# Kernel tuning notes

Measured on AMD Instinct MI355X. Metric: run time of the kernel, lower is better.

The kernel has to match this reference:

```python
import jax, jax.numpy as jnp
import numpy as np

B, NA, NB, E = 2, 256, 256, 512
H1, H2 = 300, 100


def setup_inputs() -> dict:
    key = jax.random.key(0)
    ks = jax.random.split(key, 16)

    def n(k, shape, scale=1.0):
        return jax.random.normal(k, shape, dtype=jnp.float32) * scale

    z = lambda shape: jnp.zeros(shape, jnp.float32)
    return {
        "action_embedding": n(ks[0], (B, E, NA)),
        "anchor_embedding": n(ks[1], (B, E, NB)),
        "action_points": n(ks[2], (B, 3, NA)),
        "anchor_points": n(ks[3], (B, 3, NB)),
        # pairwise MLP kernel params: 2E -> 300 -> 100 -> 1
        "mlp_W1": n(ks[4], (2 * E, H1), (2 * E) ** -0.5),
        "mlp_b1": z((H1,)),
        "mlp_W2": n(ks[5], (H1, H2), H1 ** -0.5),
        "mlp_b2": z((H2,)),
        "mlp_W3": n(ks[6], (H2, 1), H2 ** -0.5),
        "mlp_b3": z((1,)),
        # PointNet [512,64,64,64,128,512] (1x1 convs) + Conv1d(512,1,bias=False)
        "pn_W0": n(ks[7], (64, 512), 512 ** -0.5),
        "pn_b0": z((64,)),
        "pn_W1": n(ks[8], (64, 64), 64 ** -0.5),
        "pn_b1": z((64,)),
        "pn_W2": n(ks[9], (64, 64), 64 ** -0.5),
        "pn_b2": z((64,)),
        "pn_W3": n(ks[10], (128, 64), 64 ** -0.5),
        "pn_b3": z((128,)),
        "pn_W4": n(ks[11], (512, 128), 128 ** -0.5),
        "pn_b4": z((512,)),
        "head_W": n(ks[12], (1, 512), 512 ** -0.5),
    }


def reference(action_embedding, anchor_embedding, action_points, anchor_points,
              mlp_W1, mlp_b1, mlp_W2, mlp_b2, mlp_W3, mlp_b3,
              pn_W0, pn_b0, pn_W1, pn_b1, pn_W2, pn_b2, pn_W3, pn_b3,
              pn_W4, pn_b4, head_W):
    P_A = action_points.transpose(0, 2, 1)      # (B, NA, 3)
    P_B = anchor_points.transpose(0, 2, 1)      # (B, NB, 3)
    Phi_A = action_embedding.transpose(0, 2, 1)  # (B, NA, E)
    Phi_B = anchor_embedding.transpose(0, 2, 1)  # (B, NB, E)
    Ed = Phi_A.shape[-1]

    # --- symmetric pairwise MLP kernel: softplus((mlp(cat(a,b)) + mlp(cat(b,a))) / 2) ---
    # First Linear layer is split so the O(NA*NB*2E) concat is never materialized:
    # cat(a,b) @ W1 == a @ W1[:E] + b @ W1[E:]
    W1a, W1b = mlp_W1[:Ed], mlp_W1[Ed:]

    def mlp_tail(h):  # h: (B, NA, NB, H1) pre-activation of layer 1
        h = jax.nn.relu(h)
        h = jax.nn.relu(h @ mlp_W2 + mlp_b2)
        return (h @ mlp_W3 + mlp_b3)[..., 0]  # (B, NA, NB)

    hA_a = Phi_A @ W1a  # (B, NA, H1)
    hA_b = Phi_A @ W1b
    hB_a = Phi_B @ W1a  # (B, NB, H1)
    hB_b = Phi_B @ W1b
    v1 = mlp_tail(hA_a[:, :, None, :] + hB_b[:, None, :, :] + mlp_b1)  # mlp(cat(x1,x2))
    v2 = mlp_tail(hB_a[:, None, :, :] + hA_b[:, :, None, :] + mlp_b1)  # mlp(cat(x2,x1))
    R_est = jax.nn.softplus((v1 + v2) * 0.5)  # (B, NA, NB) estimated distances

    # --- weighted multilateration (estimate_p), vectorized over (B, NA) ---
    # Linearized LS: ||p||^2 - 2 q_k^T p = r_k^2 - ||q_k||^2; subtract weighted means
    # to eliminate ||p||^2, then solve 3x3 weighted normal equations per action point.
    w = jnp.ones(P_B.shape[:2], R_est.dtype)            # (B, NB) uniform weights (last_attn=False)
    wsum = w.sum(-1, keepdims=True)                      # (B, 1)
    qbar = (w[..., None] * P_B).sum(1) / wsum            # (B, 3)
    bvec = (P_B ** 2).sum(-1)[:, None, :] - R_est ** 2   # (B, NA, NB)
    bbar = (w[:, None, :] * bvec).sum(-1) / wsum         # (B, NA)
    Amat = 2.0 * (P_B - qbar[:, None, :])                # (B, NB, 3)
    yvec = bvec - bbar[..., None]                        # (B, NA, NB)
    M = jnp.einsum('bki,bk,bkj->bij', Amat, w, Amat)     # (B, 3, 3)
    rhs = jnp.einsum('bki,bk,bak->bai', Amat, w, yvec)   # (B, NA, 3)
    P_A_B_pred = jnp.linalg.solve(M[:, None], rhs[..., None])[..., 0]  # (B, NA, 3)

    flow = (P_A_B_pred - P_A).transpose(0, 2, 1)         # (B, 3, NA)

    # --- PointNet flow-weight head (1x1 convs + ReLU, final conv no bias) ---
    x = action_embedding                                  # (B, 512, NA)
    for Wc, bc in ((pn_W0, pn_b0), (pn_W1, pn_b1), (pn_W2, pn_b2),
                   (pn_W3, pn_b3), (pn_W4, pn_b4)):
        x = jax.nn.relu(jnp.einsum('oi,bin->bon', Wc, x) + bc[None, :, None])
    weight = jnp.einsum('oi,bin->bon', head_W, x)        # (B, 1, NA)

    full_flow = jnp.concatenate([flow, weight], axis=1)  # (B, 4, NA)
    return full_flow
```

## Files before the change

### kernel.cpp

```cpp
#include <hip/hip_runtime.h>
#include <hip/hip_bf16.h>
#include <hip/hip_fp16.h>

typedef float f32x4 __attribute__((ext_vector_type(4)));
typedef float f32x16 __attribute__((ext_vector_type(16)));
typedef short s16x8 __attribute__((ext_vector_type(8)));
typedef _Float16 f16x8 __attribute__((ext_vector_type(8)));

#define OFF_EMBT   0u
#define OFF_W1T    1048576u
#define OFF_W2TSW  1662976u
#define OFF_W0BF   1740800u
#define OFF_HA     1806336u
#define OFF_R2     3051520u
#define OFF_PNPK   3575808u
#define WS_TOTAL   3739648u

__device__ __forceinline__ int pack_bf2(float a, float b) {
  __hip_bfloat162 h = __float22bfloat162_rn(make_float2(a, b));
  int r; __builtin_memcpy(&r, &h, 4); return r;
}
__device__ __forceinline__ unsigned pack_f16_2(float a, float b) {
  __half2 h = __float22half2_rn(make_float2(a, b));
  unsigned r; __builtin_memcpy(&r, &h, 4); return r;
}
__device__ __forceinline__ unsigned short bf16u(float f) {
  __hip_bfloat16 h = __float2bfloat16(f);
  unsigned short u; __builtin_memcpy(&u, &h, 2); return u;
}
template<int CTRL>
__device__ __forceinline__ float dpp_add(float x) {
  int xi; __builtin_memcpy(&xi, &x, 4);
  int yi = __builtin_amdgcn_update_dpp(0, xi, CTRL, 0xf, 0xf, true);
  float y; __builtin_memcpy(&y, &yi, 4);
  return x + y;
}
__device__ __forceinline__ float swz_xor16(float x) {
  int xi; __builtin_memcpy(&xi, &x, 4);
  int yi = __builtin_amdgcn_ds_swizzle(xi, 0x401f);
  float y; __builtin_memcpy(&y, &yi, 4);
  return y;
}

__global__ __launch_bounds__(256) void ka_prep(
    const float* __restrict__ act_emb, const float* __restrict__ anc_emb,
    const float* __restrict__ W1, const float* __restrict__ W2,
    const float* __restrict__ W0pn,
    const float* __restrict__ pnW1, const float* __restrict__ pnW2,
    const float* __restrict__ pnW3, const float* __restrict__ pnW4,
    char* __restrict__ ws)
{
  __hip_bfloat16* embT  = (__hip_bfloat16*)(ws + OFF_EMBT);
  __hip_bfloat16* W1T   = (__hip_bfloat16*)(ws + OFF_W1T);
  unsigned short* W2Tsw = (unsigned short*)(ws + OFF_W2TSW);
  unsigned short* W0bf  = (unsigned short*)(ws + OFF_W0BF);
  __shared__ float tile[64][65];
  int blk = blockIdx.x, t = threadIdx.x;
  if (blk < 128) {
    int b = blk >> 6, emb = (blk >> 5) & 1, ntile = (blk >> 3) & 3, etile = blk & 7;
    const float* src = emb ? anc_emb : act_emb;
    int e0 = etile * 64, n0 = ntile * 64;
    int rr = t >> 6, cc = t & 63;
    #pragma unroll
    for (int it2 = 0; it2 < 16; ++it2) {
      int e_l = rr * 16 + it2;
      tile[e_l][cc] = src[(size_t)(b * 512 + e0 + e_l) * 256 + n0 + cc];
    }
    __syncthreads();
    int n_l = t >> 2, eq = t & 3;
    unsigned int* dst = (unsigned int*)(embT + ((size_t)((b * 2 + emb) * 256 + n0 + n_l)) * 512 + e0 + eq * 16);
    #pragma unroll
    for (int kk = 0; kk < 8; ++kk)
      dst[kk] = (unsigned)pack_bf2(tile[eq * 16 + 2 * kk][n_l], tile[eq * 16 + 2 * kk + 1][n_l]);
  } else if (blk < 208) {
    int id = blk - 128;
    int half = id / 40; int rem = id % 40; int et = rem / 5; int ct = rem % 5;
    int e0 = et * 64, c0 = ct * 64;
    int rr = t >> 6, cc = t & 63;
    #pragma unroll
    for (int it2 = 0; it2 < 16; ++it2) {
      int e_l = rr * 16 + it2;
      int c = c0 + cc;
      tile[e_l][cc] = (c < 300) ? W1[(size_t)(half * 512 + e0 + e_l) * 300 + c] : 0.f;
    }
    __syncthreads();
    int c_l = t >> 2, eq = t & 3;
    if (c0 + c_l < 300) {
      unsigned int* dst = (unsigned int*)(W1T + ((size_t)(half * 300 + c0 + c_l)) * 512 + e0 + eq * 16);
      #pragma unroll
      for (int kk = 0; kk < 8; ++kk)
        dst[kk] = (unsigned)pack_bf2(tile[eq * 16 + 2 * kk][c_l], tile[eq * 16 + 2 * kk + 1][c_l]);
    }
  } else if (blk < 227) {
    int idx = (blk - 208) * 256 + t;
    int lane = idx & 63; int ntks = idx >> 6; int nt = ntks & 3; int ks = ntks >> 2;
    int n = nt * 32 + (lane & 31);
    int kb = ks * 16 + (lane >> 5) * 8;
    unsigned int q[4];
    #pragma unroll
    for (int jj = 0; jj < 4; ++jj) {
      int k0 = kb + jj * 2, k1 = kb + jj * 2 + 1;
      float f0 = (n < 100 && k0 < 300) ? W2[(size_t)k0 * 100 + n] : 0.f;
      float f1 = (n < 100 && k1 < 300) ? W2[(size_t)k1 * 100 + n] : 0.f;
      q[jj] = pack_f16_2(f0, f1);
    }
    ((uint4*)W2Tsw)[idx] = make_uint4(q[0], q[1], q[2], q[3]);
  } else if (blk < 243) {
    int idx = (blk - 227) * 256 + t;
    const float* s = W0pn + (size_t)idx * 8;
    ((uint4*)W0bf)[idx] = make_uint4(
        (unsigned)pack_bf2(s[0], s[1]), (unsigned)pack_bf2(s[2], s[3]),
        (unsigned)pack_bf2(s[4], s[5]), (unsigned)pack_bf2(s[6], s[7]));
  } else if (blk < 247) {
    int idx = (blk - 243) * 256 + t;
    _Float16* haf = (_Float16*)(ws + OFF_HA);
    #pragma unroll
    for (int u2 = 0; u2 < 2; ++u2) {
      int unit = idx * 2 + u2;
      int combo = unit >> 5, row = unit & 31;
      size_t off = (((size_t)combo * 19 + 18) << 9) + (1 << 8) + (row << 3) + 4;
      unsigned* p = (unsigned*)(haf + off);
      p[0] = 0u; p[1] = 0u;
    }
  } else {
    int idx = (blk - 247) * 256 + t;
    const float* s;
    if (idx < 512)       s = pnW1 + (size_t)idx * 8;
    else if (idx < 1024) s = pnW2 + (size_t)(idx - 512) * 8;
    else if (idx < 2048) s = pnW3 + (size_t)(idx - 1024) * 8;
    else                 s = pnW4 + (size_t)(idx - 2048) * 8;
    unsigned short* pnPK = (unsigned short*)(ws + OFF_PNPK);
    ((uint4*)pnPK)[idx] = make_uint4(
        (unsigned)pack_bf2(s[0], s[1]), (unsigned)pack_bf2(s[2], s[3]),
        (unsigned)pack_bf2(s[4], s[5]), (unsigned)pack_bf2(s[6], s[7]));
  }
}

template<int K, int NT>
__device__ __forceinline__ void pn_layer(unsigned short* xb, const unsigned short* __restrict__ Wp,
                                         const float* __restrict__ bias, int wv, int l, int g)
{
  constexpr int NN = NT / 4;
  f32x4 z = {0.f, 0.f, 0.f, 0.f};
  f32x4 acc[NN];
  #pragma unroll
  for (int nn = 0; nn < NN; ++nn) acc[nn] = z;
  #pragma unroll
  for (int nn = 0; nn < NN; ++nn) {
    int o = (wv + nn * 4) * 16 + l;
    const unsigned short* wr0 = Wp + (size_t)o * K;
    #pragma unroll
    for (int ks = 0; ks < K / 32; ++ks) {
      int koff = ks * 32 + g * 8;
      s16x8 bfr = *(const s16x8*)(wr0 + koff);
      s16x8 a0 = *(const s16x8*)(xb + (size_t)l * 520 + koff);
      acc[nn] = __builtin_amdgcn_mfma_f32_16x16x32_bf16(a0, bfr, acc[nn], 0, 0, 0);
    }
  }
  __syncthreads();
  #pragma unroll
  for (int nn = 0; nn < NN; ++nn) {
    int chan = (wv + nn * 4) * 16 + l;
    float bv = bias[chan];
    #pragma unroll
    for (int r = 0; r < 4; ++r)
      xb[(size_t)(g * 4 + r) * 520 + chan] = bf16u(fmaxf(acc[nn][r] + bv, 0.f));
  }
  __syncthreads();
}

__global__ __launch_bounds__(256) void k1_ha(
    const __hip_bfloat16* __restrict__ embT, const __hip_bfloat16* __restrict__ W1T,
    const float* __restrict__ b1, _Float16* __restrict__ ha_f,
    const unsigned short* __restrict__ W0bf, const unsigned short* __restrict__ pnPK,
    const float* __restrict__ pnB0, const float* __restrict__ pnB1,
    const float* __restrict__ pnB2, const float* __restrict__ pnB3,
    const float* __restrict__ pnB4,
    const float* __restrict__ headW, float* __restrict__ out)
{
  __shared__ unsigned short xbuf[16 * 520];
  int blk = blockIdx.x, t = threadIdx.x;
  int wv = t >> 6, lane = t & 63, l = lane & 15, g = lane >> 4;
  if (blk < 320) {
    int b = blk / 160; int r = blk % 160; int emb = r / 80; r %= 80;
    int mch = r / 5; int nch = r % 5;
    int m0 = mch * 16;
    const unsigned short* Ap = (const unsigned short*)embT +
        ((size_t)((b * 2 + emb) * 256 + m0 + l)) * 512;
    const unsigned short* Wp = (const unsigned short*)W1T;
    f32x4 z = {0.f, 0.f, 0.f, 0.f};
    f32x4 acc[2] = {z, z};
    for (int ks = 0; ks < 16; ++ks) {
      int k0 = ks * 32 + g * 8;
      s16x8 af = *(const s16x8*)(Ap + k0);
      #pragma unroll
      for (int q = 0; q < 2; ++q) {
        int c = nch * 120 + (wv * 2 + q) * 16 + l;
        s16x8 bf = {0, 0, 0, 0, 0, 0, 0, 0};
        if (c < 600) bf = *(const s16x8*)(Wp + (size_t)c * 512 + k0);
        acc[q] = __builtin_amdgcn_mfma_f32_16x16x32_bf16(af, bf, acc[q], 0, 0, 0);
      }
    }
    #pragma unroll
    for (int q = 0; q < 2; ++q) {
      int cl = (wv * 2 + q) * 16 + l;
      int c = nch * 120 + cl;
      if (cl < 120 && c < 600) {
        int half = (c >= 300) ? 1 : 0;
        int cc = c - half * 300;
        float bias = (emb == 0) ? b1[cc] : 0.f;
        int d = emb * 2 + half;
        int ksf = cc >> 4, hi2 = (cc >> 3) & 1, e = cc & 7;
        #pragma unroll
        for (int r2 = 0; r2 < 4; ++r2) {
          int i = m0 + g * 4 + r2;
          size_t off = (((((size_t)(b * 4 + d)) * 8 + (i >> 5)) * 19 + ksf) << 9)
                     + (hi2 << 8) + ((i & 31) << 3) + e;
          ha_f[off] = (_Float16)__float2half_rn(acc[q][r2] + bias);
        }
      }
    }
  } else {
    int pn = blk - 320;
    int b_pn = pn >> 4, n0 = (pn & 15) * 16;
    unsigned short* xb = xbuf;
    {
      const unsigned short* A0 = (const unsigned short*)embT + ((size_t)(b_pn * 2 * 256 + n0)) * 512;
      f32x4 acc0 = {0.f, 0.f, 0.f, 0.f};
      int o = wv * 16 + l;
      const unsigned short* w0r = W0bf + (size_t)o * 512;
      #pragma unroll
      for (int ks = 0; ks < 16; ++ks) {
        int koff = ks * 32 + g * 8;
        s16x8 bfr = *(const s16x8*)(w0r + koff);
        s16x8 a0 = *(const s16x8*)(A0 + (size_t)l * 512 + koff);
        acc0 = __builtin_amdgcn_mfma_f32_16x16x32_bf16(a0, bfr, acc0, 0, 0, 0);
      }
      float bv = pnB0[o];
      #pragma unroll
      for (int r2 = 0; r2 < 4; ++r2)
        xb[(size_t)(g * 4 + r2) * 520 + o] = bf16u(fmaxf(acc0[r2] + bv, 0.f));
      __syncthreads();
    }
    pn_layer<64, 4>(xb, pnPK, pnB1, wv, l, g);
    pn_layer<64, 4>(xb, pnPK + 4096, pnB2, wv, l, g);
    pn_layer<64, 8>(xb, pnPK + 8192, pnB3, wv, l, g);
    pn_layer<128, 32>(xb, pnPK + 16384, pnB4, wv, l, g);
    {
      int p_l = t >> 4, os = t & 15;
      const unsigned short* row = xb + (size_t)p_l * 520 + os * 32;
      float s = 0.f;
      #pragma unroll
      for (int c = 0; c < 32; ++c) {
        unsigned int u = ((unsigned int)row[c]) << 16;
        float xv; __builtin_memcpy(&xv, &u, 4);
        s += xv * headW[os * 32 + c];
      }
      s += __shfl_xor(s, 1); s += __shfl_xor(s, 2);
      s += __shfl_xor(s, 4); s += __shfl_xor(s, 8);
      if (os == 0) out[(size_t)(b_pn * 4 + 3) * 256 + n0 + p_l] = s;
    }
  }
}

__global__ __launch_bounds__(512, 2) void k2_main(
    const _Float16* __restrict__ haF, const unsigned short* __restrict__ W2Tsw,
    const float* __restrict__ b2g, const float* __restrict__ W3g, const float* __restrict__ b3g,
    float* __restrict__ R2)
{
  __shared__ int4 w2s[4864];
  __shared__ float ex[4][2][2][16];
  int blkp = blockIdx.x, t = threadIdx.x;
  int blk = (blkp & 7) * 64 + (blkp >> 3);
  int wv = t >> 6, lane = t & 63, col = lane & 31, hi = lane >> 5;
  int jl = wv & 3, nh = wv >> 2;
  int u = blk; int b = u >> 8; u &= 255; int it = u >> 5; int jtp = u & 31;
  int i0 = it * 32;
  int j0 = jtp * 8 + jl * 2;
  {
    const int4* w2g = (const int4*)W2Tsw;
    #pragma unroll
    for (int q = 0; q < 9; ++q) { int idx = t + q * 512; w2s[idx] = w2g[idx]; }
    { int idx = t + 9 * 512; if (idx < 4864) w2s[idx] = w2g[idx]; }
  }
  const _Float16* pA0 = haF + ((((size_t)(b * 4 + 0)) * 8 + it) * 19) * 512 + lane * 8;
  const _Float16* pA1 = haF + ((((size_t)(b * 4 + 1)) * 8 + it) * 19) * 512 + lane * 8;
  const _Float16* pB00 = haF + ((((size_t)(b * 4 + 3)) * 8 + (j0 >> 5)) * 19) * 512
                         + (hi * 32 + (j0 & 31)) * 8;
  const _Float16* pB10 = haF + ((((size_t)(b * 4 + 2)) * 8 + (j0 >> 5)) * 19) * 512
                         + (hi * 32 + (j0 & 31)) * 8;
  f16x8 a0c = *(const f16x8*)(pA0);
  f16x8 a1c = *(const f16x8*)(pA1);
  f16x8 b00c = *(const f16x8*)(pB00);
  f16x8 b01c = *(const f16x8*)(pB00 + 8);
  f16x8 b10c = *(const f16x8*)(pB10);
  f16x8 b11c = *(const f16x8*)(pB10 + 8);
  __syncthreads();

  const f16x8 zf = {0, 0, 0, 0, 0, 0, 0, 0};
  f32x16 z16;
  #pragma unroll
  for (int q = 0; q < 16; ++q) z16[q] = 0.f;
  f32x16 aJ0D0N0 = z16, aJ0D0N1 = z16, aJ0D1N0 = z16, aJ0D1N1 = z16;
  f32x16 aJ1D0N0 = z16, aJ1D0N1 = z16, aJ1D1N0 = z16, aJ1D1N1 = z16;

  #pragma unroll 1
  for (int ks = 0; ks < 19; ++ks) {
    f16x8 a0n, a1n, b00n, b01n, b10n, b11n;
    if (ks < 18) {
      int ko = (ks + 1) * 512;
      a0n = *(const f16x8*)(pA0 + ko);
      a1n = *(const f16x8*)(pA1 + ko);
      b00n = *(const f16x8*)(pB00 + ko);
      b01n = *(const f16x8*)(pB00 + ko + 8);
      b10n = *(const f16x8*)(pB10 + ko);
      b11n = *(const f16x8*)(pB10 + ko + 8);
    } else { a0n = a0c; a1n = a1c; b00n = b00c; b01n = b01c; b10n = b10c; b11n = b11c; }
    f16x8 af00 = __builtin_elementwise_max(a0c + b00c, zf);
    f16x8 af01 = __builtin_elementwise_max(a0c + b01c, zf);
    f16x8 af10 = __builtin_elementwise_max(a1c + b10c, zf);
    f16x8 af11 = __builtin_elementwise_max(a1c + b11c, zf);
    const int4* wp = &w2s[ks * 256 + nh * 128 + lane];
    f16x8 wf0 = *(const f16x8*)(wp);
    f16x8 wf1 = *(const f16x8*)(wp + 64);
    aJ0D0N0 = __builtin_amdgcn_mfma_f32_32x32x16_f16(af00, wf0, aJ0D0N0, 0, 0, 0);
    aJ1D0N0 = __builtin_amdgcn_mfma_f32_32x32x16_f16(af01, wf0, aJ1D0N0, 0, 0, 0);
    aJ0D1N0 = __builtin_amdgcn_mfma_f32_32x32x16_f16(af10, wf0, aJ0D1N0, 0, 0, 0);
    aJ1D1N0 = __builtin_amdgcn_mfma_f32_32x32x16_f16(af11, wf0, aJ1D1N0, 0, 0, 0);
    aJ0D0N1 = __builtin_amdgcn_mfma_f32_32x32x16_f16(af00, wf1, aJ0D0N1, 0, 0, 0);
    aJ1D0N1 = __builtin_amdgcn_mfma_f32_32x32x16_f16(af01, wf1, aJ1D0N1, 0, 0, 0);
    aJ0D1N1 = __builtin_amdgcn_mfma_f32_32x32x16_f16(af10, wf1, aJ0D1N1, 0, 0, 0);
    aJ1D1N1 = __builtin_amdgcn_mfma_f32_32x32x16_f16(af11, wf1, aJ1D1N1, 0, 0, 0);
    a0c = a0n; a1c = a1n; b00c = b00n; b01c = b01n; b10c = b10n; b11c = b11n;
  }
  {
    float w3v[2], b2v[2];
    #pragma unroll
    for (int nt2 = 0; nt2 < 2; ++nt2) {
      int n = (nh * 2 + nt2) * 32 + col;
      w3v[nt2] = (n < 100) ? W3g[n] : 0.f;
      b2v[nt2] = (n < 100) ? b2g[n] : 0.f;
    }
    float b3 = b3g[0];
    float m0 = 0.f, m1 = 0.f;
    #pragma unroll
    for (int r = 0; r < 16; ++r) {
      float x0 = fmaxf(aJ0D0N0[r] + b2v[0], 0.f) * w3v[0] + fmaxf(aJ0D0N1[r] + b2v[1], 0.f) * w3v[1]
               + fmaxf(aJ0D1N0[r] + b2v[0], 0.f) * w3v[0] + fmaxf(aJ0D1N1[r] + b2v[1], 0.f) * w3v[1];
      float x1 = fmaxf(aJ1D0N0[r] + b2v[0], 0.f) * w3v[0] + fmaxf(aJ1D0N1[r] + b2v[1], 0.f) * w3v[1]
               + fmaxf(aJ1D1N0[r] + b2v[0], 0.f) * w3v[0] + fmaxf(aJ1D1N1[r] + b2v[1], 0.f) * w3v[1];
      x0 = dpp_add<0xB1>(x0); x1 = dpp_add<0xB1>(x1);
      x0 = dpp_add<0x4E>(x0); x1 = dpp_add<0x4E>(x1);
      x0 = dpp_add<0x141>(x0); x1 = dpp_add<0x141>(x1);
      x0 = dpp_add<0x140>(x0); x1 = dpp_add<0x140>(x1);
      x0 += swz_xor16(x0); x1 += swz_xor16(x1);
      if (col == r) { m0 = x0; m1 = x1; }
    }
    __syncthreads();
    if (nh == 1 && col < 16) { ex[jl][0][hi][col] = m0; ex[jl][1][hi][col] = m1; }
    __syncthreads();
    if (nh == 0 && col < 16) {
      float t0 = m0 + ex[jl][0][hi][col];
      float t1 = m1 + ex[jl][1][hi][col];
      float S0 = 0.5f * t0 + b3;
      float S1 = 0.5f * t1 + b3;
      float R0 = (S0 > 20.f) ? S0 : log1pf(expf(S0));
      float R1 = (S1 > 20.f) ? S1 : log1pf(expf(S1));
      int il = (col & 3) + 8 * (col >> 2) + 4 * hi;
      float* dst = &R2[((size_t)(b * 256 + i0 + il)) * 256 + j0];
      dst[0] = R0 * R0;
      dst[1] = R1 * R1;
    }
  }
}

__device__ __forceinline__ float block_sum(float v, float* redbuf, int t) {
  #pragma unroll
  for (int m = 1; m < 64; m <<= 1) v += __shfl_xor(v, m);
  __syncthreads();
  if ((t & 63) == 0) redbuf[t >> 6] = v;
  __syncthreads();
  return redbuf[0] + redbuf[1] + redbuf[2] + redbuf[3];
}

__global__ __launch_bounds__(256) void k3_solve(
    const float* __restrict__ anc_pts, const float* __restrict__ act_pts,
    const float* __restrict__ R2, float* __restrict__ out)
{
  __shared__ float Ax[256], Ay[256], Az[256];
  __shared__ float redbuf[4];
  int blk = blockIdx.x, t = threadIdx.x;
  int b = blk >> 3, ic = blk & 7;
  int k = t;
  float px = anc_pts[(size_t)(b * 3 + 0) * 256 + k];
  float py = anc_pts[(size_t)(b * 3 + 1) * 256 + k];
  float pz = anc_pts[(size_t)(b * 3 + 2) * 256 + k];
  float qx = block_sum(px, redbuf, t) * (1.f / 256.f);
  float qy = block_sum(py, redbuf, t) * (1.f / 256.f);
  float qz = block_sum(pz, redbuf, t) * (1.f / 256.f);
  float ax = 2.f * (px - qx), ay = 2.f * (py - qy), az = 2.f * (pz - qz);
  float p2 = px * px + py * py + pz * pz;
  Ax[k] = ax; Ay[k] = ay; Az[k] = az;
  float mxx = block_sum(ax * ax, redbuf, t);
  float mxy = block_sum(ax * ay, redbuf, t);
  float mxz = block_sum(ax * az, redbuf, t);
  float myy = block_sum(ay * ay, redbuf, t);
  float myz = block_sum(ay * az, redbuf, t);
  float mzz = block_sum(az * az, redbuf, t);
  float c0x = block_sum(ax * p2, redbuf, t);
  float c0y = block_sum(ay * p2, redbuf, t);
  float c0z = block_sum(az * p2, redbuf, t);
  __syncthreads();
  float det = mxx * (myy * mzz - myz * myz) - mxy * (mxy * mzz - myz * mxz) + mxz * (mxy * myz - myy * mxz);
  float idet = 1.f / det;
  float i00 = (myy * mzz - myz * myz) * idet;
  float i01 = (mxz * myz - mxy * mzz) * idet;
  float i02 = (mxy * myz - mxz * myy) * idet;
  float i11 = (mxx * mzz - mxz * mxz) * idet;
  float i12 = (mxy * mxz - mxx * myz) * idet;
  float i22 = (mxx * myy - mxy * mxy) * idet;
  int il = t >> 3, ksq = t & 7;
  int i = ic * 32 + il;
  const float* rrow = R2 + ((size_t)(b * 256 + i)) * 256;
  float r0 = 0.f, r1 = 0.f, r2 = 0.f;
  #pragma unroll
  for (int kk = 0; kk < 8; ++kk) {
    int kb = ksq * 32 + kk * 4;
    f32x4 rv = *(const f32x4*)(rrow + kb);
    r0 += Ax[kb] * rv.x + Ax[kb + 1] * rv.y + Ax[kb + 2] * rv.z + Ax[kb + 3] * rv.w;
    r1 += Ay[kb] * rv.x + Ay[kb + 1] * rv.y + Ay[kb + 2] * rv.z + Ay[kb + 3] * rv.w;
    r2 += Az[kb] * rv.x + Az[kb + 1] * rv.y + Az[kb + 2] * rv.z + Az[kb + 3] * rv.w;
  }
  r0 += __shfl_xor(r0, 1); r0 += __shfl_xor(r0, 2); r0 += __shfl_xor(r0, 4);
  r1 += __shfl_xor(r1, 1); r1 += __shfl_xor(r1, 2); r1 += __shfl_xor(r1, 4);
  r2 += __shfl_xor(r2, 1); r2 += __shfl_xor(r2, 2); r2 += __shfl_xor(r2, 4);
  if (ksq == 0) {
    float hx = c0x - r0, hy = c0y - r1, hz = c0z - r2;
    float x0 = i00 * hx + i01 * hy + i02 * hz;
    float x1 = i01 * hx + i11 * hy + i12 * hz;
    float x2 = i02 * hx + i12 * hy + i22 * hz;
    out[(size_t)(b * 4 + 0) * 256 + i] = x0 - act_pts[(size_t)(b * 3 + 0) * 256 + i];
    out[(size_t)(b * 4 + 1) * 256 + i] = x1 - act_pts[(size_t)(b * 3 + 1) * 256 + i];
    out[(size_t)(b * 4 + 2) * 256 + i] = x2 - act_pts[(size_t)(b * 3 + 2) * 256 + i];
  }
}

extern "C" void kernel_launch(void* const* d_in, const int* in_sizes, int n_in,
                              void* d_out, int out_size, void* d_ws, size_t ws_size,
                              hipStream_t stream)
{
  const float* act_emb = (const float*)d_in[0];
  const float* anc_emb = (const float*)d_in[1];
  const float* act_pts = (const float*)d_in[2];
  const float* anc_pts = (const float*)d_in[3];
  const float* W1  = (const float*)d_in[4];
  const float* b1  = (const float*)d_in[5];
  const float* W2  = (const float*)d_in[6];
  const float* b2  = (const float*)d_in[7];
  const float* W3  = (const float*)d_in[8];
  const float* b3  = (const float*)d_in[9];
  const float* pnW0 = (const float*)d_in[10];
  const float* pnB0 = (const float*)d_in[11];
  const float* pnW1 = (const float*)d_in[12];
  const float* pnB1 = (const float*)d_in[13];
  const float* pnW2 = (const float*)d_in[14];
  const float* pnB2 = (const float*)d_in[15];
  const float* pnW3 = (const float*)d_in[16];
  const float* pnB3 = (const float*)d_in[17];
  const float* pnW4 = (const float*)d_in[18];
  const float* pnB4 = (const float*)d_in[19];
  const float* headW = (const float*)d_in[20];
  char* ws = (char*)d_ws;
  __hip_bfloat16* embT  = (__hip_bfloat16*)(ws + OFF_EMBT);
  __hip_bfloat16* W1T   = (__hip_bfloat16*)(ws + OFF_W1T);
  unsigned short* W2Tsw = (unsigned short*)(ws + OFF_W2TSW);
  unsigned short* W0bf  = (unsigned short*)(ws + OFF_W0BF);
  unsigned short* pnPK  = (unsigned short*)(ws + OFF_PNPK);
  _Float16* ha_f = (_Float16*)(ws + OFF_HA);
  float* R2ws  = (float*)(ws + OFF_R2);
  float* outp  = (float*)d_out;

  ka_prep<<<287, 256, 0, stream>>>(act_emb, anc_emb, W1, W2, pnW0,
                                   pnW1, pnW2, pnW3, pnW4, ws);
  k1_ha<<<352, 256, 0, stream>>>(embT, W1T, b1, ha_f, W0bf, pnPK,
                                 pnB0, pnB1, pnB2, pnB3, pnB4,
                                 headW, outp);
  k2_main<<<512, 512, 0, stream>>>(ha_f, W2Tsw, b2, W3, b3, R2ws);
  k3_solve<<<16, 256, 0, stream>>>(anc_pts, act_pts, R2ws, outp);
}
```

Baseline: 157.5 us.

## Shrink k2 blocks, stream W2 from global, widen k3 grid, reorder k1 blocks

k2_main moves from 512-thread blocks that stage all of W2 in LDS and compute two j columns per wave to 256-thread blocks that each compute one j column per wave. W2 fragments are now prefetched straight from global memory, with no LDS staging. This quadruples the grid to 2048 blocks and cuts the per-thread accumulators from 8 to 4. k3_solve is split into 64 blocks covering 8 rows each, and k1 now schedules the PointNet blocks first. The aim is more occupancy and parallelism and less LDS setup, at the cost of more global/L2 traffic for W2 and reloading the A/B fragments across more blocks.

```diff
diff --git a/kernel.cpp b/kernel.cpp
--- a/kernel.cpp
+++ b/kernel.cpp
@@ -181,8 +181,9 @@
   __shared__ unsigned short xbuf[16 * 520];
   int blk = blockIdx.x, t = threadIdx.x;
   int wv = t >> 6, lane = t & 63, l = lane & 15, g = lane >> 4;
-  if (blk < 320) {
-    int b = blk / 160; int r = blk % 160; int emb = r / 80; r %= 80;
+  if (blk >= 32) {
+    int gb = blk - 32;
+    int b = gb / 160; int r = gb % 160; int emb = r / 80; r %= 80;
     int mch = r / 5; int nch = r % 5;
     int m0 = mch * 16;
     const unsigned short* Ap = (const unsigned short*)embT +
@@ -221,7 +222,7 @@
       }
     }
   } else {
-    int pn = blk - 320;
+    int pn = blk;
     int b_pn = pn >> 4, n0 = (pn & 15) * 16;
     unsigned short* xb = xbuf;
     {
@@ -263,113 +264,88 @@
   }
 }
 
-__global__ __launch_bounds__(512, 2) void k2_main(
+__global__ __launch_bounds__(256, 3) void k2_main(
     const _Float16* __restrict__ haF, const unsigned short* __restrict__ W2Tsw,
     const float* __restrict__ b2g, const float* __restrict__ W3g, const float* __restrict__ b3g,
     float* __restrict__ R2)
 {
-  __shared__ int4 w2s[4864];
-  __shared__ float ex[4][2][2][16];
+  __shared__ float ex[2][2][16];
   int blkp = blockIdx.x, t = threadIdx.x;
-  int blk = (blkp & 7) * 64 + (blkp >> 3);
+  int blk = (blkp & 7) * 256 + (blkp >> 3);
   int wv = t >> 6, lane = t & 63, col = lane & 31, hi = lane >> 5;
-  int jl = wv & 3, nh = wv >> 2;
-  int u = blk; int b = u >> 8; u &= 255; int it = u >> 5; int jtp = u & 31;
+  int jl = wv & 1, nh = wv >> 1;
+  int u = blk; int b = u >> 10; u &= 1023; int it = u >> 7; int jt = u & 127;
   int i0 = it * 32;
-  int j0 = jtp * 8 + jl * 2;
-  {
-    const int4* w2g = (const int4*)W2Tsw;
-    #pragma unroll
-    for (int q = 0; q < 9; ++q) { int idx = t + q * 512; w2s[idx] = w2g[idx]; }
-    { int idx = t + 9 * 512; if (idx < 4864) w2s[idx] = w2g[idx]; }
-  }
+  int j = jt * 2 + jl;
+  const int4* w2g = (const int4*)W2Tsw + nh * 128 + lane;
   const _Float16* pA0 = haF + ((((size_t)(b * 4 + 0)) * 8 + it) * 19) * 512 + lane * 8;
   const _Float16* pA1 = haF + ((((size_t)(b * 4 + 1)) * 8 + it) * 19) * 512 + lane * 8;
-  const _Float16* pB00 = haF + ((((size_t)(b * 4 + 3)) * 8 + (j0 >> 5)) * 19) * 512
-                         + (hi * 32 + (j0 & 31)) * 8;
-  const _Float16* pB10 = haF + ((((size_t)(b * 4 + 2)) * 8 + (j0 >> 5)) * 19) * 512
-                         + (hi * 32 + (j0 & 31)) * 8;
+  const _Float16* pB0 = haF + ((((size_t)(b * 4 + 3)) * 8 + (j >> 5)) * 19) * 512
+                        + (hi * 32 + (j & 31)) * 8;
+  const _Float16* pB1 = haF + ((((size_t)(b * 4 + 2)) * 8 + (j >> 5)) * 19) * 512
+                        + (hi * 32 + (j & 31)) * 8;
   f16x8 a0c = *(const f16x8*)(pA0);
   f16x8 a1c = *(const f16x8*)(pA1);
-  f16x8 b00c = *(const f16x8*)(pB00);
-  f16x8 b01c = *(const f16x8*)(pB00 + 8);
-  f16x8 b10c = *(const f16x8*)(pB10);
-  f16x8 b11c = *(const f16x8*)(pB10 + 8);
-  __syncthreads();
+  f16x8 b0c = *(const f16x8*)(pB0);
+  f16x8 b1c = *(const f16x8*)(pB1);
+  f16x8 w0c = *(const f16x8*)(w2g);
+  f16x8 w1c = *(const f16x8*)(w2g + 64);
 
   const f16x8 zf = {0, 0, 0, 0, 0, 0, 0, 0};
   f32x16 z16;
   #pragma unroll
   for (int q = 0; q < 16; ++q) z16[q] = 0.f;
-  f32x16 aJ0D0N0 = z16, aJ0D0N1 = z16, aJ0D1N0 = z16, aJ0D1N1 = z16;
-  f32x16 aJ1D0N0 = z16, aJ1D0N1 = z16, aJ1D1N0 = z16, aJ1D1N1 = z16;
+  f32x16 a00 = z16, a01 = z16, a10 = z16, a11 = z16;
 
   #pragma unroll 1
   for (int ks = 0; ks < 19; ++ks) {
-    f16x8 a0n, a1n, b00n, b01n, b10n, b11n;
+    f16x8 a0n, a1n, b0n, b1n, w0n, w1n;
     if (ks < 18) {
       int ko = (ks + 1) * 512;
       a0n = *(const f16x8*)(pA0 + ko);
       a1n = *(const f16x8*)(pA1 + ko);
-      b00n = *(const f16x8*)(pB00 + ko);
-      b01n = *(const f16x8*)(pB00 + ko + 8);
-      b10n = *(const f16x8*)(pB10 + ko);
-      b11n = *(const f16x8*)(pB10 + ko + 8);
-    } else { a0n = a0c; a1n = a1c; b00n = b00c; b01n = b01c; b10n = b10c; b11n = b11c; }
-    f16x8 af00 = __builtin_elementwise_max(a0c + b00c, zf);
-    f16x8 af01 = __builtin_elementwise_max(a0c + b01c, zf);
-    f16x8 af10 = __builtin_elementwise_max(a1c + b10c, zf);
-    f16x8 af11 = __builtin_elementwise_max(a1c + b11c, zf);
-    const int4* wp = &w2s[ks * 256 + nh * 128 + lane];
-    f16x8 wf0 = *(const f16x8*)(wp);
-    f16x8 wf1 = *(const f16x8*)(wp + 64);
-    aJ0D0N0 = __builtin_amdgcn_mfma_f32_32x32x16_f16(af00, wf0, aJ0D0N0, 0, 0, 0);
-    aJ1D0N0 = __builtin_amdgcn_mfma_f32_32x32x16_f16(af01, wf0, aJ1D0N0, 0, 0, 0);
-    aJ0D1N0 = __builtin_amdgcn_mfma_f32_32x32x16_f16(af10, wf0, aJ0D1N0, 0, 0, 0);
-    aJ1D1N0 = __builtin_amdgcn_mfma_f32_32x32x16_f16(af11, wf0, aJ1D1N0, 0, 0, 0);
-    aJ0D0N1 = __builtin_amdgcn_mfma_f32_32x32x16_f16(af00, wf1, aJ0D0N1, 0, 0, 0);
-    aJ1D0N1 = __builtin_amdgcn_mfma_f32_32x32x16_f16(af01, wf1, aJ1D0N1, 0, 0, 0);
-    aJ0D1N1 = __builtin_amdgcn_mfma_f32_32x32x16_f16(af10, wf1, aJ0D1N1, 0, 0, 0);
-    aJ1D1N1 = __builtin_amdgcn_mfma_f32_32x32x16_f16(af11, wf1, aJ1D1N1, 0, 0, 0);
-    a0c = a0n; a1c = a1n; b00c = b00n; b01c = b01n; b10c = b10n; b11c = b11n;
+      b0n = *(const f16x8*)(pB0 + ko);
+      b1n = *(const f16x8*)(pB1 + ko);
+      const int4* wn = w2g + (ks + 1) * 256;
+      w0n = *(const f16x8*)(wn);
+      w1n = *(const f16x8*)(wn + 64);
+    } else { a0n = a0c; a1n = a1c; b0n = b0c; b1n = b1c; w0n = w0c; w1n = w1c; }
+    f16x8 af0 = __builtin_elementwise_max(a0c + b0c, zf);
+    f16x8 af1 = __builtin_elementwise_max(a1c + b1c, zf);
+    a00 = __builtin_amdgcn_mfma_f32_32x32x16_f16(af0, w0c, a00, 0, 0, 0);
+    a10 = __builtin_amdgcn_mfma_f32_32x32x16_f16(af1, w0c, a10, 0, 0, 0);
+    a01 = __builtin_amdgcn_mfma_f32_32x32x16_f16(af0, w1c, a01, 0, 0, 0);
+    a11 = __builtin_amdgcn_mfma_f32_32x32x16_f16(af1, w1c, a11, 0, 0, 0);
+    a0c = a0n; a1c = a1n; b0c = b0n; b1c = b1n; w0c = w0n; w1c = w1n;
   }
   {
-    float w3v[2], b2v[2];
-    #pragma unroll
-    for (int nt2 = 0; nt2 < 2; ++nt2) {
-      int n = (nh * 2 + nt2) * 32 + col;
-      w3v[nt2] = (n < 100) ? W3g[n] : 0.f;
-      b2v[nt2] = (n < 100) ? b2g[n] : 0.f;
-    }
+    int n0 = (nh * 2) * 32 + col, n1 = n0 + 32;
+    float w3v0 = (n0 < 100) ? W3g[n0] : 0.f;
+    float w3v1 = (n1 < 100) ? W3g[n1] : 0.f;
+    float b2v0 = (n0 < 100) ? b2g[n0] : 0.f;
+    float b2v1 = (n1 < 100) ? b2g[n1] : 0.f;
     float b3 = b3g[0];
-    float m0 = 0.f, m1 = 0.f;
+    float mine = 0.f;
     #pragma unroll
     for (int r = 0; r < 16; ++r) {
-      float x0 = fmaxf(aJ0D0N0[r] + b2v[0], 0.f) * w3v[0] + fmaxf(aJ0D0N1[r] + b2v[1], 0.f) * w3v[1]
-               + fmaxf(aJ0D1N0[r] + b2v[0], 0.f) * w3v[0] + fmaxf(aJ0D1N1[r] + b2v[1], 0.f) * w3v[1];
-      float x1 = fmaxf(aJ1D0N0[r] + b2v[0], 0.f) * w3v[0] + fmaxf(aJ1D0N1[r] + b2v[1], 0.f) * w3v[1]
-               + fmaxf(aJ1D1N0[r] + b2v[0], 0.f) * w3v[0] + fmaxf(aJ1D1N1[r] + b2v[1], 0.f) * w3v[1];
-      x0 = dpp_add<0xB1>(x0); x1 = dpp_add<0xB1>(x1);
-      x0 = dpp_add<0x4E>(x0); x1 = dpp_add<0x4E>(x1);
-      x0 = dpp_add<0x141>(x0); x1 = dpp_add<0x141>(x1);
-      x0 = dpp_add<0x140>(x0); x1 = dpp_add<0x140>(x1);
-      x0 += swz_xor16(x0); x1 += swz_xor16(x1);
-      if (col == r) { m0 = x0; m1 = x1; }
+      float x = fmaxf(a00[r] + b2v0, 0.f) * w3v0 + fmaxf(a01[r] + b2v1, 0.f) * w3v1
+              + fmaxf(a10[r] + b2v0, 0.f) * w3v0 + fmaxf(a11[r] + b2v1, 0.f) * w3v1;
+      x = dpp_add<0xB1>(x);
+      x = dpp_add<0x4E>(x);
+      x = dpp_add<0x141>(x);
+      x = dpp_add<0x140>(x);
+      x += swz_xor16(x);
+      if (col == r) mine = x;
     }
     __syncthreads();
-    if (nh == 1 && col < 16) { ex[jl][0][hi][col] = m0; ex[jl][1][hi][col] = m1; }
+    if (nh == 1 && col < 16) ex[jl][hi][col] = mine;
     __syncthreads();
     if (nh == 0 && col < 16) {
-      float t0 = m0 + ex[jl][0][hi][col];
-      float t1 = m1 + ex[jl][1][hi][col];
-      float S0 = 0.5f * t0 + b3;
-      float S1 = 0.5f * t1 + b3;
-      float R0 = (S0 > 20.f) ? S0 : log1pf(expf(S0));
-      float R1 = (S1 > 20.f) ? S1 : log1pf(expf(S1));
+      float tot = mine + ex[jl][hi][col];
+      float S = 0.5f * tot + b3;
+      float Rr = (S > 20.f) ? S : log1pf(expf(S));
       int il = (col & 3) + 8 * (col >> 2) + 4 * hi;
-      float* dst = &R2[((size_t)(b * 256 + i0 + il)) * 256 + j0];
-      dst[0] = R0 * R0;
-      dst[1] = R1 * R1;
+      R2[((size_t)(b * 256 + i0 + il)) * 256 + j] = Rr * Rr;
     }
   }
 }
@@ -390,7 +366,7 @@
   __shared__ float Ax[256], Ay[256], Az[256];
   __shared__ float redbuf[4];
   int blk = blockIdx.x, t = threadIdx.x;
-  int b = blk >> 3, ic = blk & 7;
+  int b = blk >> 5, ic = blk & 31;
   int k = t;
   float px = anc_pts[(size_t)(b * 3 + 0) * 256 + k];
   float py = anc_pts[(size_t)(b * 3 + 1) * 256 + k];
@@ -419,21 +395,24 @@
   float i11 = (mxx * mzz - mxz * mxz) * idet;
   float i12 = (mxy * mxz - mxx * myz) * idet;
   float i22 = (mxx * myy - mxy * mxy) * idet;
-  int il = t >> 3, ksq = t & 7;
-  int i = ic * 32 + il;
+  int il = t >> 5, ksq = t & 31;
+  int i = ic * 8 + il;
   const float* rrow = R2 + ((size_t)(b * 256 + i)) * 256;
   float r0 = 0.f, r1 = 0.f, r2 = 0.f;
   #pragma unroll
-  for (int kk = 0; kk < 8; ++kk) {
-    int kb = ksq * 32 + kk * 4;
+  for (int kk = 0; kk < 2; ++kk) {
+    int kb = ksq * 8 + kk * 4;
     f32x4 rv = *(const f32x4*)(rrow + kb);
     r0 += Ax[kb] * rv.x + Ax[kb + 1] * rv.y + Ax[kb + 2] * rv.z + Ax[kb + 3] * rv.w;
     r1 += Ay[kb] * rv.x + Ay[kb + 1] * rv.y + Ay[kb + 2] * rv.z + Ay[kb + 3] * rv.w;
     r2 += Az[kb] * rv.x + Az[kb + 1] * rv.y + Az[kb + 2] * rv.z + Az[kb + 3] * rv.w;
   }
   r0 += __shfl_xor(r0, 1); r0 += __shfl_xor(r0, 2); r0 += __shfl_xor(r0, 4);
+  r0 += __shfl_xor(r0, 8); r0 += __shfl_xor(r0, 16);
   r1 += __shfl_xor(r1, 1); r1 += __shfl_xor(r1, 2); r1 += __shfl_xor(r1, 4);
+  r1 += __shfl_xor(r1, 8); r1 += __shfl_xor(r1, 16);
   r2 += __shfl_xor(r2, 1); r2 += __shfl_xor(r2, 2); r2 += __shfl_xor(r2, 4);
+  r2 += __shfl_xor(r2, 8); r2 += __shfl_xor(r2, 16);
   if (ksq == 0) {
     float hx = c0x - r0, hy = c0y - r1, hz = c0z - r2;
     float x0 = i00 * hx + i01 * hy + i02 * hz;
@@ -485,6 +464,6 @@
   k1_ha<<<352, 256, 0, stream>>>(embT, W1T, b1, ha_f, W0bf, pnPK,
                                  pnB0, pnB1, pnB2, pnB3, pnB4,
                                  headW, outp);
-  k2_main<<<512, 512, 0, stream>>>(ha_f, W2Tsw, b2, W3, b3, R2ws);
-  k3_solve<<<16, 256, 0, stream>>>(anc_pts, act_pts, R2ws, outp);
-}
+  k2_main<<<2048, 256, 0, stream>>>(ha_f, W2Tsw, b2, W3, b3, R2ws);
+  k3_solve<<<64, 256, 0, stream>>>(anc_pts, act_pts, R2ws, outp);
+}
```

Measured after the change: 155.4 us. Within noise of the previous version (-1.3%).
